# Kernel tuning notes

Measured on AMD Instinct MI355X. Metric: run time of the kernel, lower is better.

## Reference

```python
import jax, jax.numpy as jnp
import numpy as np

N = 100000      # nodes
E = 1600000     # edges
G = 64          # graphs in batch
IN_CH = 2
HID = 64
HEADS = 4
TASKS = 2
NEG_SLOPE = 0.2  # PyG GATConv default leaky-relu slope


def gat_conv(x, src, dst, W, att_src, att_dst, bias, heads, out_ch, concat):
    """PyG-style GATConv (eval mode, self-loops added).
    x: [N, F_in]; src/dst: [Et]; W: [F_in, heads*out_ch];
    att_src/att_dst: [heads, out_ch]; bias: [heads*out_ch] or [out_ch]."""
    n = x.shape[0]
    xh = (x @ W).reshape(n, heads, out_ch)            # [N,H,C]
    a_src = jnp.einsum('nhc,hc->nh', xh, att_src)     # [N,H]
    a_dst = jnp.einsum('nhc,hc->nh', xh, att_dst)     # [N,H]
    e = a_src[src] + a_dst[dst]                       # [Et,H]
    e = jax.nn.leaky_relu(e, NEG_SLOPE)
    # segment softmax over incoming edges of each destination node
    e_max = jax.ops.segment_max(e, dst, num_segments=n)
    alpha = jnp.exp(e - e_max[dst])
    denom = jax.ops.segment_sum(alpha, dst, num_segments=n)
    alpha = alpha / denom[dst]                        # [Et,H]
    msg = xh[src] * alpha[:, :, None]                 # [Et,H,C]
    out = jax.ops.segment_sum(msg, dst, num_segments=n)  # [N,H,C]
    if concat:
        return out.reshape(n, heads * out_ch) + bias
    return out.mean(axis=1) + bias


def setup_inputs() -> dict:
    key = jax.random.key(0)
    ks = jax.random.split(key, 13)
    s = 0.1
    return {
        'x': jax.random.normal(ks[0], (N, IN_CH), dtype=jnp.float32),
        'edge_index': jax.random.randint(ks[1], (2, E), 0, N, dtype=jnp.int64)
            if jax.config.jax_enable_x64 else jax.random.randint(ks[1], (2, E), 0, N, dtype=jnp.int32),
        'batch': jnp.sort(jax.random.randint(ks[2], (N,), 0, G, dtype=jnp.int32)),
        'W1': jax.random.normal(ks[3], (IN_CH, HEADS * HID), dtype=jnp.float32) * s,
        'att_src1': jax.random.normal(ks[4], (HEADS, HID), dtype=jnp.float32) * s,
        'att_dst1': jax.random.normal(ks[5], (HEADS, HID), dtype=jnp.float32) * s,
        'b1': jnp.zeros((HEADS * HID,), dtype=jnp.float32),
        'W2': jax.random.normal(ks[6], (HEADS * HID, HID), dtype=jnp.float32) * s,
        'att_src2': jax.random.normal(ks[7], (1, HID), dtype=jnp.float32) * s,
        'att_dst2': jax.random.normal(ks[8], (1, HID), dtype=jnp.float32) * s,
        'b2': jnp.zeros((HID,), dtype=jnp.float32),
        'W_lin': jax.random.normal(ks[9], (HID, TASKS), dtype=jnp.float32) * s,
        'b_lin': jnp.zeros((TASKS,), dtype=jnp.float32),
    }


def reference(x, edge_index, batch, W1, att_src1, att_dst1, b1,
              W2, att_src2, att_dst2, b2, W_lin, b_lin):
    n = x.shape[0]
    # PyG GATConv adds self-loops by default
    loops = jnp.arange(n, dtype=edge_index.dtype)
    src = jnp.concatenate([edge_index[0], loops])
    dst = jnp.concatenate([edge_index[1], loops])

    h = jax.nn.elu(gat_conv(x, src, dst, W1, att_src1, att_dst1, b1,
                            HEADS, HID, concat=True))        # [N, 256]
    # dropout is identity in eval mode
    h = jax.nn.elu(gat_conv(h, src, dst, W2, att_src2, att_dst2, b2,
                            1, HID, concat=False))           # [N, 64]

    # global mean pool over graphs
    sums = jax.ops.segment_sum(h, batch, num_segments=G)     # [G, 64]
    counts = jax.ops.segment_sum(jnp.ones((n,), h.dtype), batch, num_segments=G)
    pooled = sums / jnp.maximum(counts, 1.0)[:, None]

    return pooled @ W_lin + b_lin                            # [G, 2]
```

## Files before the change

### kernel.cpp

```cpp
#include <hip/hip_runtime.h>
#include <hip/hip_fp16.h>
#include <math.h>

#define HID 64
#define HEADS 4
#define GR 64
#define NEG 0.2f
#define NBKT_MAX 512
#define BK_SH 8
#define PART_T 2048

typedef _Float16 f16x8 __attribute__((ext_vector_type(8)));
typedef float    f32x4 __attribute__((ext_vector_type(4)));

__device__ __forceinline__ float lrelu(float v){ return v > 0.f ? v : NEG * v; }
__device__ __forceinline__ float elu_(float v){ return v > 0.f ? v : __expf(v) - 1.f; }

__global__ void k_init(float* sums, int* counts, int* bcnt,
                       const float* __restrict__ W1, const float* __restrict__ as1,
                       const float* __restrict__ ad1, float* cvec){
    int i = blockIdx.x * blockDim.x + threadIdx.x;
    if (i < GR * HID) sums[i] = 0.f;
    if (i < GR) counts[i] = 0;
    if (i < NBKT_MAX) bcnt[i] = 0;
    if (blockIdx.x == 0 && threadIdx.x < 64){
        int lane = threadIdx.x;
#pragma unroll
        for (int h = 0; h < HEADS; h++){
            int j = h * HID + lane;
            float s0 = W1[j]       * as1[j];
            float s1 = W1[256 + j] * as1[j];
            float d0 = W1[j]       * ad1[j];
            float d1 = W1[256 + j] * ad1[j];
#pragma unroll
            for (int off = 32; off; off >>= 1){
                s0 += __shfl_xor(s0, off, 64);
                s1 += __shfl_xor(s1, off, 64);
                d0 += __shfl_xor(d0, off, 64);
                d1 += __shfl_xor(d1, off, 64);
            }
            if (lane == 0){
                cvec[h] = s0; cvec[4 + h] = s1; cvec[8 + h] = d0; cvec[12 + h] = d1;
            }
        }
    }
}

__global__ void k_w2frag(const float* __restrict__ W2, uint4* __restrict__ w2frag){
    int t = blockIdx.x * blockDim.x + threadIdx.x;
    if (t >= 2048) return;
    int lane = t & 63, c = (t >> 6) & 3, s = t >> 8;
    union { uint4 u; _Float16 h[8]; } o;
#pragma unroll
    for (int e = 0; e < 8; e++){
        int k = 32 * s + 4 * (lane >> 4) + (e & 3) + 16 * (e >> 2);
        int col = 16 * c + (lane & 15);
        o.h[e] = (_Float16)W2[k * 64 + col];
    }
    w2frag[t] = o.u;
}

__global__ void k_histB(const int* __restrict__ dst, int E, int* bcnt){
    __shared__ int bh[NBKT_MAX];
    for (int b = threadIdx.x; b < NBKT_MAX; b += blockDim.x) bh[b] = 0;
    __syncthreads();
    int stride = gridDim.x * blockDim.x;
    for (int i = blockIdx.x * blockDim.x + threadIdx.x; i < E; i += stride)
        atomicAdd(&bh[dst[i] >> BK_SH], 1);
    __syncthreads();
    for (int b = threadIdx.x; b < NBKT_MAX; b += blockDim.x)
        if (bh[b]) atomicAdd(&bcnt[b], bh[b]);
}

__global__ void k_bscan(const int* __restrict__ bcnt, int* bbase, int* bcursor){
    __shared__ int sh[NBKT_MAX];
    int t = threadIdx.x;
    int v = bcnt[t];
    sh[t] = v;
    __syncthreads();
    for (int off = 1; off < NBKT_MAX; off <<= 1){
        int u = (t >= off) ? sh[t - off] : 0;
        __syncthreads();
        sh[t] += u;
        __syncthreads();
    }
    bbase[t] = sh[t] - v;
    bcursor[t] = sh[t] - v;
    if (t == NBKT_MAX - 1) bbase[NBKT_MAX] = sh[t];
}

__global__ void __launch_bounds__(256)
k_part(const int* __restrict__ src, const int* __restrict__ dst, int E,
       int* bcursor, unsigned int* __restrict__ tmp){
    __shared__ int bh[NBKT_MAX];
    __shared__ int gbl[NBKT_MAX];
    int tid = threadIdx.x;
    int base = blockIdx.x * PART_T;
    for (int b = tid; b < NBKT_MAX; b += 256) bh[b] = 0;
    __syncthreads();
#pragma unroll
    for (int r = 0; r < PART_T / 256; r++){
        int i = base + r * 256 + tid;
        if (i < E) atomicAdd(&bh[dst[i] >> BK_SH], 1);
    }
    __syncthreads();
    for (int b = tid; b < NBKT_MAX; b += 256){
        int c = bh[b];
        gbl[b] = c ? atomicAdd(&bcursor[b], c) : 0;
        bh[b] = 0;
    }
    __syncthreads();
#pragma unroll
    for (int r = 0; r < PART_T / 256; r++){
        int i = base + r * 256 + tid;
        if (i < E){
            int s = src[i], d = dst[i];
            int b = d >> BK_SH;
            int rank = atomicAdd(&bh[b], 1);
            tmp[(size_t)(gbl[b] + rank)] =
                ((unsigned)(d & ((1 << BK_SH) - 1)) << 17) | (unsigned)s;
        }
    }
}

__global__ void __launch_bounds__(256)
k_csr2(const unsigned int* __restrict__ tmp, const int* __restrict__ bbase,
       int N, int Et, int* __restrict__ offs, int* __restrict__ ssrc){
    __shared__ int degl[256];
    __shared__ int rc[256];
    __shared__ int scan[256];
    __shared__ int ofl[256];
    int b = blockIdx.x, tid = threadIdx.x;
    int n0 = b << BK_SH;
    int nloc = min(256, N - n0);
    degl[tid] = 0; rc[tid] = 0;
    __syncthreads();
    int beg = bbase[b], cnt = bbase[b + 1] - beg;
    for (int i = tid; i < cnt; i += 256)
        atomicAdd(&degl[tmp[beg + i] >> 17], 1);
    __syncthreads();
    int v = (tid < nloc) ? degl[tid] + 1 : 0;
    scan[tid] = v;
    __syncthreads();
    for (int off = 1; off < 256; off <<= 1){
        int u = (tid >= off) ? scan[tid - off] : 0;
        __syncthreads();
        scan[tid] += u;
        __syncthreads();
    }
    int base = beg + n0;
    if (tid < nloc){
        int o = base + scan[tid] - v;
        ofl[tid] = o;
        offs[n0 + tid] = o;
        ssrc[o] = n0 + tid;
    }
    if (b == 0 && tid == 0) offs[N] = Et;
    __syncthreads();
    for (int i = tid; i < cnt; i += 256){
        unsigned int e = tmp[beg + i];
        int dloc = (int)(e >> 17);
        int s = (int)(e & 0x1FFFFu);
        int pos = ofl[dloc] + 1 + atomicAdd(&rc[dloc], 1);
        ssrc[pos] = s;
    }
}

__global__ void k_agg1s(const float* __restrict__ x, const int* __restrict__ offs,
                        const int* __restrict__ ssrc, const float* __restrict__ cvec,
                        int N, float4* Sa, float4* Sb, float4* Sc){
    int n = blockIdx.x * blockDim.x + threadIdx.x;
    if (n >= N) return;
    float4 cs0 = ((const float4*)cvec)[0];
    float4 cs1 = ((const float4*)cvec)[1];
    float4 cd0 = ((const float4*)cvec)[2];
    float4 cd1 = ((const float4*)cvec)[3];
    float c0[4] = {cs0.x, cs0.y, cs0.z, cs0.w};
    float c1[4] = {cs1.x, cs1.y, cs1.z, cs1.w};
    float2 xn = ((const float2*)x)[n];
    float ad[4] = {xn.x*cd0.x + xn.y*cd1.x, xn.x*cd0.y + xn.y*cd1.y,
                   xn.x*cd0.z + xn.y*cd1.z, xn.x*cd0.w + xn.y*cd1.w};
    float A0[4] = {0,0,0,0}, A1[4] = {0,0,0,0}, D[4] = {0,0,0,0};
    int beg = offs[n], end = offs[n + 1];
    int j = beg;
    for (; j + 8 <= end; j += 8){
        int si[8];
#pragma unroll
        for (int u = 0; u < 8; u++) si[u] = ssrc[j + u];
        float2 xs[8];
#pragma unroll
        for (int u = 0; u < 8; u++) xs[u] = ((const float2*)x)[si[u]];
#pragma unroll
        for (int h = 0; h < HEADS; h++){
#pragma unroll
            for (int u = 0; u < 8; u++){
                float w = __expf(lrelu(xs[u].x * c0[h] + xs[u].y * c1[h] + ad[h]));
                A0[h] += w * xs[u].x;
                A1[h] += w * xs[u].y;
                D[h]  += w;
            }
        }
    }
    if (j + 4 <= end){
        int si[4];
#pragma unroll
        for (int u = 0; u < 4; u++) si[u] = ssrc[j + u];
        float2 xs[4];
#pragma unroll
        for (int u = 0; u < 4; u++) xs[u] = ((const float2*)x)[si[u]];
#pragma unroll
        for (int h = 0; h < HEADS; h++){
#pragma unroll
            for (int u = 0; u < 4; u++){
                float w = __expf(lrelu(xs[u].x * c0[h] + xs[u].y * c1[h] + ad[h]));
                A0[h] += w * xs[u].x;
                A1[h] += w * xs[u].y;
                D[h]  += w;
            }
        }
        j += 4;
    }
    for (; j < end; j++){
        int s = ssrc[j];
        float2 xs = ((const float2*)x)[s];
#pragma unroll
        for (int h = 0; h < HEADS; h++){
            float e = xs.x * c0[h] + xs.y * c1[h] + ad[h];
            float w = __expf(lrelu(e));
            A0[h] += w * xs.x;
            A1[h] += w * xs.y;
            D[h]  += w;
        }
    }
    Sa[n] = make_float4(A0[0], A0[1], A0[2], A0[3]);
    Sb[n] = make_float4(A1[0], A1[1], A1[2], A1[3]);
    Sc[n] = make_float4(D[0],  D[1],  D[2],  D[3]);
}

__global__ void __launch_bounds__(256)
k_h1f16(const float* __restrict__ Saf, const float* __restrict__ Sbf,
        const float* __restrict__ Scf, const float* __restrict__ W1,
        const float* __restrict__ b1, int N, _Float16* __restrict__ h1){
    int tid = blockIdx.x * blockDim.x + threadIdx.x;
    int n = tid >> 6, lane = tid & 63;
    if (n >= N) return;
    int k0 = lane * 4;
    int head = lane >> 4;
    float a0 = Saf[n * 4 + head];
    float a1 = Sbf[n * 4 + head];
    float rd = 1.0f / Scf[n * 4 + head];
    float4 w0 = *(const float4*)(W1 + k0);
    float4 w1 = *(const float4*)(W1 + 256 + k0);
    float4 bv = *(const float4*)(b1 + k0);
    union { uint2 u; _Float16 h[4]; } o;
    o.h[0] = (_Float16)elu_((a0 * w0.x + a1 * w1.x) * rd + bv.x);
    o.h[1] = (_Float16)elu_((a0 * w0.y + a1 * w1.y) * rd + bv.y);
    o.h[2] = (_Float16)elu_((a0 * w0.z + a1 * w1.z) * rd + bv.z);
    o.h[3] = (_Float16)elu_((a0 * w0.w + a1 * w1.w) * rd + bv.w);
    ((uint2*)h1)[(size_t)n * 64 + lane] = o.u;
}

__global__ void __launch_bounds__(256)
k_mfma(const _Float16* __restrict__ h1, const uint4* __restrict__ w2frag,
       const float* __restrict__ as2, const float* __restrict__ ad2,
       int N, __half* __restrict__ xh2, float* __restrict__ asrc,
       float* __restrict__ adst){
    __shared__ uint4 w2s[2048];
    int tid = threadIdx.x;
    for (int i = tid; i < 2048; i += 256) w2s[i] = w2frag[i];
    __syncthreads();

    int lane = tid & 63, wv = tid >> 6;
    int r = lane & 15, g = lane >> 4;
    float asw0 = as2[r], asw1 = as2[16 + r], asw2 = as2[32 + r], asw3 = as2[48 + r];
    float adw0 = ad2[r], adw1 = ad2[16 + r], adw2 = ad2[32 + r], adw3 = ad2[48 + r];

    int ntiles = (N + 15) >> 4;
    for (int t = blockIdx.x * 4 + wv; t < ntiles; t += gridDim.x * 4){
        int base = t << 4;
        int nodeA = min(base + r, N - 1);
        const _Float16* ap = h1 + (size_t)nodeA * 256 + 4 * g;
        f32x4 ac0 = {0.f,0.f,0.f,0.f}, ac1 = {0.f,0.f,0.f,0.f};
        f32x4 ac2 = {0.f,0.f,0.f,0.f}, ac3 = {0.f,0.f,0.f,0.f};
#pragma unroll
        for (int s = 0; s < 8; s++){
            uint2 lo = *(const uint2*)(ap + 32 * s);
            uint2 hi = *(const uint2*)(ap + 32 * s + 16);
            union { uint4 u; f16x8 f; } a;
            a.u = make_uint4(lo.x, lo.y, hi.x, hi.y);
            union { uint4 u; f16x8 f; } b0, b1, b2, b3;
            b0.u = w2s[(s * 4 + 0) * 64 + lane];
            b1.u = w2s[(s * 4 + 1) * 64 + lane];
            b2.u = w2s[(s * 4 + 2) * 64 + lane];
            b3.u = w2s[(s * 4 + 3) * 64 + lane];
            ac0 = __builtin_amdgcn_mfma_f32_16x16x32_f16(a.f, b0.f, ac0, 0, 0, 0);
            ac1 = __builtin_amdgcn_mfma_f32_16x16x32_f16(a.f, b1.f, ac1, 0, 0, 0);
            ac2 = __builtin_amdgcn_mfma_f32_16x16x32_f16(a.f, b2.f, ac2, 0, 0, 0);
            ac3 = __builtin_amdgcn_mfma_f32_16x16x32_f16(a.f, b3.f, ac3, 0, 0, 0);
        }
        float ps0 = 0.f, ps1 = 0.f, ps2 = 0.f, ps3 = 0.f;
        float pd0 = 0.f, pd1 = 0.f, pd2 = 0.f, pd3 = 0.f;
#pragma unroll
        for (int reg = 0; reg < 4; reg++){
            int node = base + 4 * g + reg;
            if (node < N){
                size_t rowb = (size_t)node * 64;
                xh2[rowb +      r] = __float2half(ac0[reg]);
                xh2[rowb + 16 + r] = __float2half(ac1[reg]);
                xh2[rowb + 32 + r] = __float2half(ac2[reg]);
                xh2[rowb + 48 + r] = __float2half(ac3[reg]);
            }
            float ps = ac0[reg]*asw0 + ac1[reg]*asw1 + ac2[reg]*asw2 + ac3[reg]*asw3;
            float pd = ac0[reg]*adw0 + ac1[reg]*adw1 + ac2[reg]*adw2 + ac3[reg]*adw3;
            if (reg == 0){ ps0 = ps; pd0 = pd; }
            else if (reg == 1){ ps1 = ps; pd1 = pd; }
            else if (reg == 2){ ps2 = ps; pd2 = pd; }
            else { ps3 = ps; pd3 = pd; }
        }
#pragma unroll
        for (int m = 1; m < 16; m <<= 1){
            ps0 += __shfl_xor(ps0, m, 64); pd0 += __shfl_xor(pd0, m, 64);
            ps1 += __shfl_xor(ps1, m, 64); pd1 += __shfl_xor(pd1, m, 64);
            ps2 += __shfl_xor(ps2, m, 64); pd2 += __shfl_xor(pd2, m, 64);
            ps3 += __shfl_xor(ps3, m, 64); pd3 += __shfl_xor(pd3, m, 64);
        }
        if (r == 0){
            int nb = base + 4 * g;
            if (nb     < N){ asrc[nb    ] = ps0; adst[nb    ] = pd0; }
            if (nb + 1 < N){ asrc[nb + 1] = ps1; adst[nb + 1] = pd1; }
            if (nb + 2 < N){ asrc[nb + 2] = ps2; adst[nb + 2] = pd2; }
            if (nb + 3 < N){ asrc[nb + 3] = ps3; adst[nb + 3] = pd3; }
        }
    }
}

__global__ void k_agg2p(const __half* __restrict__ xh2, const float* __restrict__ asrc,
                        const float* __restrict__ adst, const int* __restrict__ offs,
                        const int* __restrict__ ssrc, const float* __restrict__ b2,
                        const int* __restrict__ batch, int N,
                        float* sums, int* counts){
    int tid = threadIdx.x;
    int lane = tid & 63, wv = tid >> 6;
    int c = lane & 31;
    int half = lane >> 5;
    int wid = blockIdx.x * 4 + wv;
    int nw = gridDim.x * 4;
    int chunk = (N + nw - 1) / nw;
    int beg = wid * chunk, end = min(beg + chunk, N);
    if (beg >= end) return;
    const unsigned int* xrow = (const unsigned int*)xh2;
    float b2a = b2[2 * c], b2b = b2[2 * c + 1];
    float pacc0 = 0.f, pacc1 = 0.f; int pcnt = 0; int cur = batch[beg];
    for (int n = beg; n < end; n++){
        float ad = adst[n];
        float acc0 = 0.f, acc1 = 0.f, den = 0.f;
        int e0 = offs[n], e1 = offs[n + 1];
        int j = e0;
        for (; j + 8 <= e1; j += 8){
            int sA = ssrc[j     + half];
            int sB = ssrc[j + 2 + half];
            int sC = ssrc[j + 4 + half];
            int sD = ssrc[j + 6 + half];
            float aA = asrc[sA], aB = asrc[sB], aC = asrc[sC], aD = asrc[sD];
            unsigned int rA = xrow[(size_t)sA * 32 + c];
            unsigned int rB = xrow[(size_t)sB * 32 + c];
            unsigned int rC = xrow[(size_t)sC * 32 + c];
            unsigned int rD = xrow[(size_t)sD * 32 + c];
            float wA = __expf(lrelu(aA + ad));
            float wB = __expf(lrelu(aB + ad));
            float wC = __expf(lrelu(aC + ad));
            float wD = __expf(lrelu(aD + ad));
            float2 fA = __half22float2(*(const __half2*)&rA);
            float2 fB = __half22float2(*(const __half2*)&rB);
            float2 fC = __half22float2(*(const __half2*)&rC);
            float2 fD = __half22float2(*(const __half2*)&rD);
            acc0 += wA * fA.x + wB * fB.x + wC * fC.x + wD * fD.x;
            acc1 += wA * fA.y + wB * fB.y + wC * fC.y + wD * fD.y;
            den  += wA + wB + wC + wD;
        }
        for (; j + 2 <= e1; j += 2){
            int s = ssrc[j + half];
            float a = asrc[s];
            unsigned int r = xrow[(size_t)s * 32 + c];
            float w = __expf(lrelu(a + ad));
            float2 f = __half22float2(*(const __half2*)&r);
            acc0 += w * f.x;
            acc1 += w * f.y;
            den  += w;
        }
        if (j < e1){
            int s = ssrc[j];
            float w = (half == 0) ? __expf(lrelu(asrc[s] + ad)) : 0.f;
            unsigned int r = xrow[(size_t)s * 32 + c];
            float2 f = __half22float2(*(const __half2*)&r);
            acc0 += w * f.x;
            acc1 += w * f.y;
            den  += w;
        }
        acc0 += __shfl_xor(acc0, 32, 64);
        acc1 += __shfl_xor(acc1, 32, 64);
        den  += __shfl_xor(den, 32, 64);
        float h2a = elu_(acc0 / den + b2a);
        float h2b = elu_(acc1 / den + b2b);
        int g = batch[n];
        if (g != cur){
            if (half == 0){
                atomicAdd(&sums[cur * HID + 2 * c    ], pacc0);
                atomicAdd(&sums[cur * HID + 2 * c + 1], pacc1);
            }
            if (lane == 0) atomicAdd(&counts[cur], pcnt);
            pacc0 = 0.f; pacc1 = 0.f; pcnt = 0; cur = g;
        }
        pacc0 += h2a; pacc1 += h2b; pcnt++;
    }
    if (half == 0){
        atomicAdd(&sums[cur * HID + 2 * c    ], pacc0);
        atomicAdd(&sums[cur * HID + 2 * c + 1], pacc1);
    }
    if (lane == 0) atomicAdd(&counts[cur], pcnt);
}

__global__ void k_final(const float* __restrict__ sums, const int* __restrict__ counts,
                        const float* __restrict__ Wl, const float* __restrict__ bl,
                        float* out){
    int t = threadIdx.x;
    if (t >= GR * 2) return;
    int g = t >> 1, task = t & 1;
    float c = (float)max(counts[g], 1);
    float acc = 0.f;
#pragma unroll
    for (int k = 0; k < HID; k++)
        acc += (sums[g * HID + k] / c) * Wl[k * 2 + task];
    out[t] = acc + bl[task];
}

extern "C" void kernel_launch(void* const* d_in, const int* in_sizes, int n_in,
                              void* d_out, int out_size, void* d_ws, size_t ws_size,
                              hipStream_t stream) {
    const float* x    = (const float*)d_in[0];
    const int*   ei   = (const int*)  d_in[1];
    const int*   batch= (const int*)  d_in[2];
    const float* W1   = (const float*)d_in[3];
    const float* as1  = (const float*)d_in[4];
    const float* ad1  = (const float*)d_in[5];
    const float* b1   = (const float*)d_in[6];
    const float* W2   = (const float*)d_in[7];
    const float* as2  = (const float*)d_in[8];
    const float* ad2  = (const float*)d_in[9];
    const float* b2   = (const float*)d_in[10];
    const float* Wl   = (const float*)d_in[11];
    const float* bl   = (const float*)d_in[12];
    float* out = (float*)d_out;

    int N  = in_sizes[0] / 2;
    int E  = in_sizes[1] / 2;
    int Et = E + N;
    const int* srcp = ei;
    const int* dstp = ei + E;

    char* p = (char*)d_ws;
    auto alloc = [&](size_t bytes)->char* {
        char* r = p; p += (bytes + 255) & ~(size_t)255; return r;
    };
    int*    offs   = (int*)   alloc((size_t)(N + 1) * 4);
    int*    bcnt   = (int*)   alloc(NBKT_MAX * 4);
    int*    bbase  = (int*)   alloc((NBKT_MAX + 1) * 4);
    int*    bcursor= (int*)   alloc(NBKT_MAX * 4);
    int*    ssrc   = (int*)   alloc((size_t)Et * 4);
    unsigned int* tmp = (unsigned int*)alloc((size_t)E * 4);
    float*  cvec   = (float*) alloc(16 * 4);
    float4* Sa     = (float4*)alloc((size_t)N * 16);
    float4* Sb     = (float4*)alloc((size_t)N * 16);
    float4* Sc     = (float4*)alloc((size_t)N * 16);
    float*  asrc2  = (float*) alloc((size_t)N * 4);
    float*  adst2  = (float*) alloc((size_t)N * 4);
    float*  sums   = (float*) alloc((size_t)GR * HID * 4);
    int*    counts = (int*)   alloc((size_t)GR * 4);
    uint4*  w2frag = (uint4*) alloc(2048 * 16);
    _Float16* h1f  = (_Float16*)alloc((size_t)N * 256 * 2);
    __half* xh2    = (__half*)alloc((size_t)N * 64 * 2);

    int nbkt = (N + 255) >> BK_SH;

    k_init  <<<16, 256, 0, stream>>>(sums, counts, bcnt, W1, as1, ad1, cvec);
    k_w2frag<<<8, 256, 0, stream>>>(W2, w2frag);
    k_histB <<<256, 256, 0, stream>>>(dstp, E, bcnt);
    k_bscan <<<1, NBKT_MAX, 0, stream>>>(bcnt, bbase, bcursor);
    k_part  <<<(E + PART_T - 1) / PART_T, 256, 0, stream>>>(srcp, dstp, E, bcursor, tmp);
    k_csr2  <<<nbkt, 256, 0, stream>>>(tmp, bbase, N, Et, offs, ssrc);

    k_agg1s <<<(N + 255) / 256, 256, 0, stream>>>(x, offs, ssrc, cvec, N, Sa, Sb, Sc);
    k_h1f16 <<<(N * 64 + 255) / 256, 256, 0, stream>>>((const float*)Sa, (const float*)Sb,
                                                       (const float*)Sc, W1, b1, N, h1f);
    k_mfma  <<<1024, 256, 0, stream>>>(h1f, w2frag, as2, ad2, N, xh2, asrc2, adst2);
    k_agg2p <<<2048, 256, 0, stream>>>(xh2, asrc2, adst2, offs, ssrc, b2,
                                       batch, N, sums, counts);
    k_final <<<1, 128, 0, stream>>>(sums, counts, Wl, bl, out);
}
```

Measured before the change: 213.6 us.

## Fuse h1 construction into MFMA kernel, merge W2 prep into histogram, deepen agg2 unroll

The layer-1 output (ELU of the attention-weighted projection) is now computed on the fly inside the MFMA GEMM kernel from the per-node Sa/Sb/Sc sums, with W1 and b1 staged in shared memory. This removes the separate k_h1f16 kernel and the N x 256 fp16 intermediate buffer, avoiding writing and re-reading about 51 MB. The W2 fragment-packing kernel is merged into the histogram kernel as extra blocks, saving one launch. The layer-2 aggregation loop is unrolled to 16 edges with batched gathers to expose more memory-level parallelism, at the cost of more registers and redundant ELU/exp work in the GEMM.

```diff
diff --git a/kernel.cpp b/kernel.cpp
--- a/kernel.cpp
+++ b/kernel.cpp
@@ -46,30 +46,32 @@
     }
 }
 
-__global__ void k_w2frag(const float* __restrict__ W2, uint4* __restrict__ w2frag){
-    int t = blockIdx.x * blockDim.x + threadIdx.x;
-    if (t >= 2048) return;
-    int lane = t & 63, c = (t >> 6) & 3, s = t >> 8;
-    union { uint4 u; _Float16 h[8]; } o;
-#pragma unroll
-    for (int e = 0; e < 8; e++){
-        int k = 32 * s + 4 * (lane >> 4) + (e & 3) + 16 * (e >> 2);
-        int col = 16 * c + (lane & 15);
-        o.h[e] = (_Float16)W2[k * 64 + col];
-    }
-    w2frag[t] = o.u;
-}
-
-__global__ void k_histB(const int* __restrict__ dst, int E, int* bcnt){
+__global__ void k_histW(const int* __restrict__ dst, int E, int* bcnt,
+                        const float* __restrict__ W2, uint4* __restrict__ w2frag){
     __shared__ int bh[NBKT_MAX];
-    for (int b = threadIdx.x; b < NBKT_MAX; b += blockDim.x) bh[b] = 0;
-    __syncthreads();
-    int stride = gridDim.x * blockDim.x;
-    for (int i = blockIdx.x * blockDim.x + threadIdx.x; i < E; i += stride)
-        atomicAdd(&bh[dst[i] >> BK_SH], 1);
-    __syncthreads();
-    for (int b = threadIdx.x; b < NBKT_MAX; b += blockDim.x)
-        if (bh[b]) atomicAdd(&bcnt[b], bh[b]);
+    if (blockIdx.x < 256){
+        for (int b = threadIdx.x; b < NBKT_MAX; b += blockDim.x) bh[b] = 0;
+        __syncthreads();
+        int stride = 256 * blockDim.x;
+        for (int i = blockIdx.x * blockDim.x + threadIdx.x; i < E; i += stride)
+            atomicAdd(&bh[dst[i] >> BK_SH], 1);
+        __syncthreads();
+        for (int b = threadIdx.x; b < NBKT_MAX; b += blockDim.x)
+            if (bh[b]) atomicAdd(&bcnt[b], bh[b]);
+    } else {
+        int t = (blockIdx.x - 256) * 256 + threadIdx.x;
+        if (t < 2048){
+            int lane = t & 63, c = (t >> 6) & 3, s = t >> 8;
+            union { uint4 u; _Float16 h[8]; } o;
+#pragma unroll
+            for (int e = 0; e < 8; e++){
+                int k = 32 * s + 4 * (lane >> 4) + (e & 3) + 16 * (e >> 2);
+                int col = 16 * c + (lane & 15);
+                o.h[e] = (_Float16)W2[k * 64 + col];
+            }
+            w2frag[t] = o.u;
+        }
+    }
 }
 
 __global__ void k_bscan(const int* __restrict__ bcnt, int* bbase, int* bcursor){
@@ -238,36 +240,21 @@
 }
 
 __global__ void __launch_bounds__(256)
-k_h1f16(const float* __restrict__ Saf, const float* __restrict__ Sbf,
-        const float* __restrict__ Scf, const float* __restrict__ W1,
-        const float* __restrict__ b1, int N, _Float16* __restrict__ h1){
-    int tid = blockIdx.x * blockDim.x + threadIdx.x;
-    int n = tid >> 6, lane = tid & 63;
-    if (n >= N) return;
-    int k0 = lane * 4;
-    int head = lane >> 4;
-    float a0 = Saf[n * 4 + head];
-    float a1 = Sbf[n * 4 + head];
-    float rd = 1.0f / Scf[n * 4 + head];
-    float4 w0 = *(const float4*)(W1 + k0);
-    float4 w1 = *(const float4*)(W1 + 256 + k0);
-    float4 bv = *(const float4*)(b1 + k0);
-    union { uint2 u; _Float16 h[4]; } o;
-    o.h[0] = (_Float16)elu_((a0 * w0.x + a1 * w1.x) * rd + bv.x);
-    o.h[1] = (_Float16)elu_((a0 * w0.y + a1 * w1.y) * rd + bv.y);
-    o.h[2] = (_Float16)elu_((a0 * w0.z + a1 * w1.z) * rd + bv.z);
-    o.h[3] = (_Float16)elu_((a0 * w0.w + a1 * w1.w) * rd + bv.w);
-    ((uint2*)h1)[(size_t)n * 64 + lane] = o.u;
-}
-
-__global__ void __launch_bounds__(256)
-k_mfma(const _Float16* __restrict__ h1, const uint4* __restrict__ w2frag,
+k_mfma(const float4* __restrict__ Sa4, const float4* __restrict__ Sb4,
+       const float4* __restrict__ Sc4, const float* __restrict__ W1,
+       const float* __restrict__ b1, const uint4* __restrict__ w2frag,
        const float* __restrict__ as2, const float* __restrict__ ad2,
        int N, __half* __restrict__ xh2, float* __restrict__ asrc,
        float* __restrict__ adst){
     __shared__ uint4 w2s[2048];
+    __shared__ float4 w1aS[64], w1bS[64], b1S[64];
     int tid = threadIdx.x;
     for (int i = tid; i < 2048; i += 256) w2s[i] = w2frag[i];
+    if (tid < 64){
+        w1aS[tid] = ((const float4*)W1)[tid];
+        w1bS[tid] = ((const float4*)W1)[tid + 64];
+        b1S[tid]  = ((const float4*)b1)[tid];
+    }
     __syncthreads();
 
     int lane = tid & 63, wv = tid >> 6;
@@ -279,24 +266,39 @@
     for (int t = blockIdx.x * 4 + wv; t < ntiles; t += gridDim.x * 4){
         int base = t << 4;
         int nodeA = min(base + r, N - 1);
-        const _Float16* ap = h1 + (size_t)nodeA * 256 + 4 * g;
+        float4 sa = Sa4[nodeA], sb = Sb4[nodeA], sc = Sc4[nodeA];
+        float rdv0 = 1.0f / sc.x, rdv1 = 1.0f / sc.y;
+        float rdv2 = 1.0f / sc.z, rdv3 = 1.0f / sc.w;
         f32x4 ac0 = {0.f,0.f,0.f,0.f}, ac1 = {0.f,0.f,0.f,0.f};
         f32x4 ac2 = {0.f,0.f,0.f,0.f}, ac3 = {0.f,0.f,0.f,0.f};
 #pragma unroll
         for (int s = 0; s < 8; s++){
-            uint2 lo = *(const uint2*)(ap + 32 * s);
-            uint2 hi = *(const uint2*)(ap + 32 * s + 16);
-            union { uint4 u; f16x8 f; } a;
-            a.u = make_uint4(lo.x, lo.y, hi.x, hi.y);
-            union { uint4 u; f16x8 f; } b0, b1, b2, b3;
-            b0.u = w2s[(s * 4 + 0) * 64 + lane];
-            b1.u = w2s[(s * 4 + 1) * 64 + lane];
-            b2.u = w2s[(s * 4 + 2) * 64 + lane];
-            b3.u = w2s[(s * 4 + 3) * 64 + lane];
-            ac0 = __builtin_amdgcn_mfma_f32_16x16x32_f16(a.f, b0.f, ac0, 0, 0, 0);
-            ac1 = __builtin_amdgcn_mfma_f32_16x16x32_f16(a.f, b1.f, ac1, 0, 0, 0);
-            ac2 = __builtin_amdgcn_mfma_f32_16x16x32_f16(a.f, b2.f, ac2, 0, 0, 0);
-            ac3 = __builtin_amdgcn_mfma_f32_16x16x32_f16(a.f, b3.f, ac3, 0, 0, 0);
+            const int head = s >> 1;
+            float A0 = head == 0 ? sa.x : head == 1 ? sa.y : head == 2 ? sa.z : sa.w;
+            float A1 = head == 0 ? sb.x : head == 1 ? sb.y : head == 2 ? sb.z : sb.w;
+            float rd = head == 0 ? rdv0 : head == 1 ? rdv1 : head == 2 ? rdv2 : rdv3;
+            int q0 = 8 * s + g;
+            float4 w0lo = w1aS[q0], w0hi = w1aS[q0 + 4];
+            float4 w1lo = w1bS[q0], w1hi = w1bS[q0 + 4];
+            float4 blo  = b1S[q0],  bhi  = b1S[q0 + 4];
+            union { uint4 u; f16x8 f; _Float16 h[8]; } a;
+            a.h[0] = (_Float16)elu_((A0 * w0lo.x + A1 * w1lo.x) * rd + blo.x);
+            a.h[1] = (_Float16)elu_((A0 * w0lo.y + A1 * w1lo.y) * rd + blo.y);
+            a.h[2] = (_Float16)elu_((A0 * w0lo.z + A1 * w1lo.z) * rd + blo.z);
+            a.h[3] = (_Float16)elu_((A0 * w0lo.w + A1 * w1lo.w) * rd + blo.w);
+            a.h[4] = (_Float16)elu_((A0 * w0hi.x + A1 * w1hi.x) * rd + bhi.x);
+            a.h[5] = (_Float16)elu_((A0 * w0hi.y + A1 * w1hi.y) * rd + bhi.y);
+            a.h[6] = (_Float16)elu_((A0 * w0hi.z + A1 * w1hi.z) * rd + bhi.z);
+            a.h[7] = (_Float16)elu_((A0 * w0hi.w + A1 * w1hi.w) * rd + bhi.w);
+            union { uint4 u; f16x8 f; } b0, b1x, b2, b3;
+            b0.u  = w2s[(s * 4 + 0) * 64 + lane];
+            b1x.u = w2s[(s * 4 + 1) * 64 + lane];
+            b2.u  = w2s[(s * 4 + 2) * 64 + lane];
+            b3.u  = w2s[(s * 4 + 3) * 64 + lane];
+            ac0 = __builtin_amdgcn_mfma_f32_16x16x32_f16(a.f, b0.f,  ac0, 0, 0, 0);
+            ac1 = __builtin_amdgcn_mfma_f32_16x16x32_f16(a.f, b1x.f, ac1, 0, 0, 0);
+            ac2 = __builtin_amdgcn_mfma_f32_16x16x32_f16(a.f, b2.f,  ac2, 0, 0, 0);
+            ac3 = __builtin_amdgcn_mfma_f32_16x16x32_f16(a.f, b3.f,  ac3, 0, 0, 0);
         }
         float ps0 = 0.f, ps1 = 0.f, ps2 = 0.f, ps3 = 0.f;
         float pd0 = 0.f, pd1 = 0.f, pd2 = 0.f, pd3 = 0.f;
@@ -356,34 +358,51 @@
         float acc0 = 0.f, acc1 = 0.f, den = 0.f;
         int e0 = offs[n], e1 = offs[n + 1];
         int j = e0;
-        for (; j + 8 <= e1; j += 8){
-            int sA = ssrc[j     + half];
-            int sB = ssrc[j + 2 + half];
-            int sC = ssrc[j + 4 + half];
-            int sD = ssrc[j + 6 + half];
-            float aA = asrc[sA], aB = asrc[sB], aC = asrc[sC], aD = asrc[sD];
-            unsigned int rA = xrow[(size_t)sA * 32 + c];
-            unsigned int rB = xrow[(size_t)sB * 32 + c];
-            unsigned int rC = xrow[(size_t)sC * 32 + c];
-            unsigned int rD = xrow[(size_t)sD * 32 + c];
-            float wA = __expf(lrelu(aA + ad));
-            float wB = __expf(lrelu(aB + ad));
-            float wC = __expf(lrelu(aC + ad));
-            float wD = __expf(lrelu(aD + ad));
-            float2 fA = __half22float2(*(const __half2*)&rA);
-            float2 fB = __half22float2(*(const __half2*)&rB);
-            float2 fC = __half22float2(*(const __half2*)&rC);
-            float2 fD = __half22float2(*(const __half2*)&rD);
-            acc0 += wA * fA.x + wB * fB.x + wC * fC.x + wD * fD.x;
-            acc1 += wA * fA.y + wB * fB.y + wC * fC.y + wD * fD.y;
-            den  += wA + wB + wC + wD;
+        for (; j + 16 <= e1; j += 16){
+            int si[8];
+#pragma unroll
+            for (int u = 0; u < 8; u++) si[u] = ssrc[j + 2 * u + half];
+            float av[8];
+#pragma unroll
+            for (int u = 0; u < 8; u++) av[u] = asrc[si[u]];
+            unsigned int rv[8];
+#pragma unroll
+            for (int u = 0; u < 8; u++) rv[u] = xrow[(size_t)si[u] * 32 + c];
+#pragma unroll
+            for (int u = 0; u < 8; u++){
+                float w = __expf(lrelu(av[u] + ad));
+                float2 f = __half22float2(*(const __half2*)&rv[u]);
+                acc0 += w * f.x;
+                acc1 += w * f.y;
+                den  += w;
+            }
+        }
+        if (j + 8 <= e1){
+            int si[4];
+#pragma unroll
+            for (int u = 0; u < 4; u++) si[u] = ssrc[j + 2 * u + half];
+            float av[4];
+#pragma unroll
+            for (int u = 0; u < 4; u++) av[u] = asrc[si[u]];
+            unsigned int rv[4];
+#pragma unroll
+            for (int u = 0; u < 4; u++) rv[u] = xrow[(size_t)si[u] * 32 + c];
+#pragma unroll
+            for (int u = 0; u < 4; u++){
+                float w = __expf(lrelu(av[u] + ad));
+                float2 f = __half22float2(*(const __half2*)&rv[u]);
+                acc0 += w * f.x;
+                acc1 += w * f.y;
+                den  += w;
+            }
+            j += 8;
         }
         for (; j + 2 <= e1; j += 2){
             int s = ssrc[j + half];
             float a = asrc[s];
-            unsigned int r = xrow[(size_t)s * 32 + c];
+            unsigned int rr = xrow[(size_t)s * 32 + c];
             float w = __expf(lrelu(a + ad));
-            float2 f = __half22float2(*(const __half2*)&r);
+            float2 f = __half22float2(*(const __half2*)&rr);
             acc0 += w * f.x;
             acc1 += w * f.y;
             den  += w;
@@ -391,8 +410,8 @@
         if (j < e1){
             int s = ssrc[j];
             float w = (half == 0) ? __expf(lrelu(asrc[s] + ad)) : 0.f;
-            unsigned int r = xrow[(size_t)s * 32 + c];
-            float2 f = __half22float2(*(const __half2*)&r);
+            unsigned int rr = xrow[(size_t)s * 32 + c];
+            float2 f = __half22float2(*(const __half2*)&rr);
             acc0 += w * f.x;
             acc1 += w * f.y;
             den  += w;
@@ -477,23 +496,20 @@
     float*  sums   = (float*) alloc((size_t)GR * HID * 4);
     int*    counts = (int*)   alloc((size_t)GR * 4);
     uint4*  w2frag = (uint4*) alloc(2048 * 16);
-    _Float16* h1f  = (_Float16*)alloc((size_t)N * 256 * 2);
     __half* xh2    = (__half*)alloc((size_t)N * 64 * 2);
 
     int nbkt = (N + 255) >> BK_SH;
 
-    k_init  <<<16, 256, 0, stream>>>(sums, counts, bcnt, W1, as1, ad1, cvec);
-    k_w2frag<<<8, 256, 0, stream>>>(W2, w2frag);
-    k_histB <<<256, 256, 0, stream>>>(dstp, E, bcnt);
-    k_bscan <<<1, NBKT_MAX, 0, stream>>>(bcnt, bbase, bcursor);
-    k_part  <<<(E + PART_T - 1) / PART_T, 256, 0, stream>>>(srcp, dstp, E, bcursor, tmp);
-    k_csr2  <<<nbkt, 256, 0, stream>>>(tmp, bbase, N, Et, offs, ssrc);
-
-    k_agg1s <<<(N + 255) / 256, 256, 0, stream>>>(x, offs, ssrc, cvec, N, Sa, Sb, Sc);
-    k_h1f16 <<<(N * 64 + 255) / 256, 256, 0, stream>>>((const float*)Sa, (const float*)Sb,
-                                                       (const float*)Sc, W1, b1, N, h1f);
-    k_mfma  <<<1024, 256, 0, stream>>>(h1f, w2frag, as2, ad2, N, xh2, asrc2, adst2);
-    k_agg2p <<<2048, 256, 0, stream>>>(xh2, asrc2, adst2, offs, ssrc, b2,
-                                       batch, N, sums, counts);
-    k_final <<<1, 128, 0, stream>>>(sums, counts, Wl, bl, out);
-}
+    k_init <<<16, 256, 0, stream>>>(sums, counts, bcnt, W1, as1, ad1, cvec);
+    k_histW<<<264, 256, 0, stream>>>(dstp, E, bcnt, W2, w2frag);
+    k_bscan<<<1, NBKT_MAX, 0, stream>>>(bcnt, bbase, bcursor);
+    k_part <<<(E + PART_T - 1) / PART_T, 256, 0, stream>>>(srcp, dstp, E, bcursor, tmp);
+    k_csr2 <<<nbkt, 256, 0, stream>>>(tmp, bbase, N, Et, offs, ssrc);
+
+    k_agg1s<<<(N + 255) / 256, 256, 0, stream>>>(x, offs, ssrc, cvec, N, Sa, Sb, Sc);
+    k_mfma <<<1024, 256, 0, stream>>>(Sa, Sb, Sc, W1, b1, w2frag, as2, ad2,
+                                      N, xh2, asrc2, adst2);
+    k_agg2p<<<2048, 256, 0, stream>>>(xh2, asrc2, adst2, offs, ssrc, b2,
+                                      batch, N, sums, counts);
+    k_final<<<1, 128, 0, stream>>>(sums, counts, Wl, bl, out);
+}
```

Measured after the change: 201.3 us. -5.8%, faster.
